# Kernel tuning notes

Hardware: AMD Instinct MI355X
Metric: run time of the kernel (lower is better)

## Reference

```python
import jax, jax.numpy as jnp
import numpy as np

B, N, IN_DIM, HID, K = 16, 1024, 512, 256, 3
ALPHA = 0.2  # leaky relu slope
NEG = -9e15  # mask value from original code (-9000000000000000.0)


def setup_inputs() -> dict:
    key = jax.random.key(0)
    ks = jax.random.split(key, 10)
    adj = (jax.random.uniform(ks[0], (B, 3, N, N)) < 0.01).astype(jnp.float32)
    inputs = jax.random.normal(ks[1], (B, N, IN_DIM), dtype=jnp.float32)
    s = 0.07
    W = jax.random.normal(ks[2], (3, K, IN_DIM, HID), dtype=jnp.float32) * s
    # attention vector a [2F,1] split into a1 (for h_i) and a2 (for h_j)
    a1 = jax.random.normal(ks[3], (3, K, HID), dtype=jnp.float32) * s
    a2 = jax.random.normal(ks[4], (3, K, HID), dtype=jnp.float32) * s
    Ww = jax.random.normal(ks[5], (HID, 100), dtype=jnp.float32) * s
    bw = jnp.zeros((100,), dtype=jnp.float32)
    Wc = jax.random.normal(ks[6], (100, 1), dtype=jnp.float32) * s
    return {"adj": adj, "inputs": inputs, "W": W, "a1": a1, "a2": a2,
            "Ww": Ww, "bw": bw, "Wc": Wc}


def _gat(adjp, inputs, W_, a1_, a2_):
    # h = X W : [B,N,F]
    h = jnp.einsum('bni,if->bnf', inputs, W_)
    # e_ij = leakyrelu(a1.h_i + a2.h_j) -- equivalent to the original
    # cat([h_i, h_j]) @ a without materializing the [B,N,N,2F] tensor
    f1 = h @ a1_  # [B,N]
    f2 = h @ a2_  # [B,N]
    e = jax.nn.leaky_relu(f1[:, :, None] + f2[:, None, :], ALPHA)
    att = jax.nn.softmax(jnp.where(adjp > 0, e, NEG), axis=2)
    # (dropout on attention is identity in eval mode)
    return jnp.einsum('bnm,bmf->bnf', att, h)


def reference(adj, inputs, W, a1, a2, Ww, bw, Wc):
    k_layers = W.shape[1]
    # powers[t] holds adj_t^(k+1) for layer k (matmuls(adj, k))
    powers = [adj[:, t] for t in range(3)]
    layer_list = []
    for k in range(k_layers):
        out = 0.0
        for t in range(3):
            out = out + _gat(powers[t], inputs, W[t, k], a1[t, k], a2[t, k])
        layer_list.append(out)
        if k + 1 < k_layers:
            powers = [jnp.matmul(p, adj[:, t]) for t, p in enumerate(powers)]
    H = jnp.stack(layer_list, axis=2)  # [B,N,K,F]
    s = jnp.tanh(H @ Ww + bw) @ Wc     # [B,N,K,1]
    vs = jax.nn.softmax(s[..., 0], axis=2)  # [B,N,K]
    return jnp.einsum('bnk,bnkf->bnf', vs, H)
```

## Files before the change

kernel.cpp:

```cpp
#include <hip/hip_runtime.h>


typedef unsigned long long u64;
typedef __attribute__((ext_vector_type(4))) float f32x4;
typedef __attribute__((ext_vector_type(8))) short bf16x8;

#define NEGF (-9.0e15f)
#define L2E 1.44269504f

__device__ __forceinline__ float fexp2(float x){
#if __has_builtin(__builtin_amdgcn_exp2f)
  return __builtin_amdgcn_exp2f(x);
#else
  return exp2f(x);
#endif
}
__device__ __forceinline__ float frcp(float x){
#if __has_builtin(__builtin_amdgcn_rcpf)
  return __builtin_amdgcn_rcpf(x);
#else
  return 1.0f/x;
#endif
}
__device__ __forceinline__ unsigned short f2bf(float x){
  union { float f; unsigned u; } a; a.f = x;
  unsigned r = a.u + 0x7FFFu + ((a.u >> 16) & 1u);
  return (unsigned short)(r >> 16);
}
__device__ __forceinline__ unsigned pack_bf16x2(float lo, float hi){
  union { float f; unsigned u; } a, b; a.f = lo; b.f = hi;
  unsigned ul = a.u + 0x8000u, uh = b.u + 0x8000u;
#if __has_builtin(__builtin_amdgcn_perm)
  return __builtin_amdgcn_perm(uh, ul, 0x07060302u);
#else
  return (ul >> 16) | (uh & 0xFFFF0000u);
#endif
}
__device__ __forceinline__ float tanh_fast(float x){
  float e = fexp2(x * 2.885390082f);
  return 1.0f - 2.0f*frcp(e + 1.0f);
}
__device__ __forceinline__ void async_cp16(void* lds, const void* g){
  __builtin_amdgcn_global_load_lds(
      (const __attribute__((address_space(1))) unsigned int*)g,
      (__attribute__((address_space(3))) unsigned int*)lds, 16, 0, 0);
}


__global__ __launch_bounds__(256) void k_prep(
    const float* __restrict__ W, const float* __restrict__ a1,
    const float* __restrict__ a2, unsigned short* __restrict__ Wb,
    const float* __restrict__ X, unsigned short* __restrict__ Xs,
    const float* __restrict__ adj, u64* __restrict__ mbA0, u64* __restrict__ mbT)
{
  if (blockIdx.x < 608) {
    int idx = blockIdx.x*256 + threadIdx.x;
    if (idx >= 64*2432) return;
    int c = idx % 2432, g = idx / 2432;
    unsigned short o[8];
    if (c < 2304) {
      int s = c >> 8, f = c & 255, t = s % 3, klq = s / 3;
      const float* wp = W + ((size_t)(t*3 + klq)*512)*256 + f;
#pragma unroll
      for (int e = 0; e < 8; ++e) o[e] = f2bf(wp[(size_t)(g*8 + e)*256]);
    } else if (c < 2322) {
      return;
    } else {
#pragma unroll
      for (int e = 0; e < 8; ++e) o[e] = 0;
    }
    ushort4 lo, hi;
    lo.x=o[0]; lo.y=o[1]; lo.z=o[2]; lo.w=o[3];
    hi.x=o[4]; hi.y=o[5]; hi.z=o[6]; hi.w=o[7];
    ushort4* dst = (ushort4*)(Wb + (size_t)idx*8);
    dst[0] = lo; dst[1] = hi;
  } else if (blockIdx.x < 896) {
    int wv = (blockIdx.x - 608)*4 + (threadIdx.x >> 6);
    int lane = threadIdx.x & 63;
    int c2 = wv >> 6, g = wv & 63;
    int s = c2 >> 1, t = s % 3, klq = s / 3;
    const float* av = ((c2 & 1) ? a2 : a1) + (t*3 + klq)*256;
    const float* wp = W + ((size_t)(t*3 + klq)*512)*256;
    float4 avv = *(const float4*)(av + lane*4);
    unsigned short o[8];
#pragma unroll
    for (int e = 0; e < 8; ++e) {
      float4 wv4 = *(const float4*)(wp + (size_t)(g*8 + e)*256 + lane*4);
      float p = wv4.x*avv.x + wv4.y*avv.y + wv4.z*avv.z + wv4.w*avv.w;
#pragma unroll
      for (int off = 32; off; off >>= 1) p += __shfl_xor(p, off);
      o[e] = f2bf(p);
    }
    if (lane == 0) {
      ushort4 lo, hi;
      lo.x=o[0]; lo.y=o[1]; lo.z=o[2]; lo.w=o[3];
      hi.x=o[4]; hi.y=o[5]; hi.z=o[6]; hi.w=o[7];
      ushort4* dst = (ushort4*)(Wb + (size_t)(g*2432 + 2304 + c2)*8);
      dst[0] = lo; dst[1] = hi;
    }
  } else if (blockIdx.x < 4992) {
    int idx = (blockIdx.x - 896)*256 + threadIdx.x;
    int bn = idx & 16383, g = idx >> 14;
    const float* xp = X + (size_t)bn*512 + g*8;
    ushort4 lo, hi;
    lo.x=f2bf(xp[0]); lo.y=f2bf(xp[1]); lo.z=f2bf(xp[2]); lo.w=f2bf(xp[3]);
    hi.x=f2bf(xp[4]); hi.y=f2bf(xp[5]); hi.z=f2bf(xp[6]); hi.w=f2bf(xp[7]);
    ushort4* dst = (ushort4*)(Xs + (size_t)idx*8);
    dst[0] = lo; dst[1] = hi;
  } else {
    int gw = (blockIdx.x - 4992)*4 + (threadIdx.x >> 6);
    int lane = threadIdx.x & 63;
#pragma unroll
    for (int r = 0; r < 2; ++r) {
      int row = gw*2 + r;
      int i = row & 1023, bt = row >> 10;
      int t = bt % 3, b = bt / 3;
      int sb = t*16 + b;
      const float* ap = adj + (size_t)row*1024 + lane;
      u64 myw = 0;
#pragma unroll
      for (int w = 0; w < 16; ++w) {
        u64 bal = __ballot(ap[w*64] > 0.0f);
        if (lane == w) myw = bal;
      }
      if (lane < 16) {
        mbA0[((size_t)sb*1024 + i)*16 + lane] = myw;
        mbT[((size_t)sb*16 + lane)*1024 + i] = myw;
      }
    }
  }
}

__global__ void k_boolmm(const u64* __restrict__ A, const u64* __restrict__ Bm,
                         u64* __restrict__ outA, u64* __restrict__ outT, int sbase)
{
  int tid = blockIdx.x*256 + threadIdx.x;
  int w = tid & 15, i = (tid >> 4) & 1023, tb = tid >> 14;
  const u64* Ar = A + ((size_t)tb*1024 + i)*16;
  const u64* Bb = Bm + (size_t)tb*16384;
  u64 acc = 0;
  for (int ww = 0; ww < 16; ++ww) {
    u64 aw = Ar[ww];
    while (aw) {
      int kk = __builtin_ctzll(aw);
      aw &= aw - 1;
      acc |= Bb[((size_t)(ww*64 + kk))*16 + w];
    }
  }
  if (outA) outA[((size_t)tb*1024 + i)*16 + w] = acc;
  int t = tb >> 4, bq = tb & 15;
  outT[(((size_t)(sbase + t)*16 + bq)*16 + w)*1024 + i] = acc;
}


__global__ __launch_bounds__(256) void k_gemm_h(
    const unsigned short* __restrict__ Xs, const unsigned short* __restrict__ Wb,
    unsigned short* __restrict__ hsw, float* __restrict__ fbuf,
    float* __restrict__ G1p, float* __restrict__ G2p)
{
  __shared__ unsigned short Asl[8*132*8 + 8];
  __shared__ unsigned short Bsl[8*132*8 + 8];
  const int tid = threadIdx.x, lane = tid & 63, wid = tid >> 6;
  int vb = blockIdx.x;
  int xc = vb & 7, mrest = vb >> 3;
  int mt = xc + 8*(mrest/19), nt = mrest % 19;
  const int M0 = mt << 7, N0 = nt << 7;
  const int wr = (wid >> 1) << 6, wc = (wid & 1) << 6;
  const int me = lane & 15;
  f32x4 acc[4][4] = {};
  for (int ks64 = 0; ks64 < 8; ++ks64) {
    __syncthreads();
#pragma unroll
    for (int c = 0; c < 4; ++c) {
      int chunk = wid*4 + c, g = chunk >> 1, hh = chunk & 1;
      int ldsoff = (g*132 + hh*64)*8;
      const unsigned short* gpA = Xs + ((size_t)(ks64*8 + g)*16384 + (M0 + hh*64 + lane))*8;
      async_cp16(Asl + ldsoff, gpA);
      const unsigned short* gpB = Wb + ((size_t)(ks64*8 + g)*2432 + (N0 + hh*64 + lane))*8;
      async_cp16(Bsl + ldsoff, gpB);
    }
    __syncthreads();
#pragma unroll
    for (int ks32 = 0; ks32 < 2; ++ks32) {
      const int kg = ks32*4 + (lane >> 4);
      bf16x8 afr[4], bfr[4];
#pragma unroll
      for (int rb = 0; rb < 4; ++rb)
        afr[rb] = *(const bf16x8*)(Asl + (kg*132 + wr + rb*16 + me)*8);
#pragma unroll
      for (int cb = 0; cb < 4; ++cb)
        bfr[cb] = *(const bf16x8*)(Bsl + (kg*132 + wc + cb*16 + me)*8);
#pragma unroll
      for (int rb = 0; rb < 4; ++rb)
#pragma unroll
        for (int cb = 0; cb < 4; ++cb)
          acc[rb][cb] = __builtin_amdgcn_mfma_f32_16x16x32_bf16(afr[rb], bfr[cb], acc[rb][cb], 0, 0, 0);
    }
  }
  const int quad = lane >> 4;
#pragma unroll
  for (int rb = 0; rb < 4; ++rb) {
    int jbase = M0 + wr + rb*16 + quad*4;
    int bidx = jbase >> 10, jn = jbase & 1023;
#pragma unroll
    for (int cb = 0; cb < 4; ++cb) {
      int c = N0 + wc + cb*16 + me;
      f32x4 v = acc[rb][cb];
      if (c < 2304) {
        int s = c >> 8, f = c & 255;
        ushort4 pk;
        pk.x = f2bf(v[0]); pk.y = f2bf(v[1]); pk.z = f2bf(v[2]); pk.w = f2bf(v[3]);
        *(ushort4*)(hsw + (size_t)s*4194304 + (size_t)bidx*262144 + ((jn>>3)*256 + f)*8 + (jn&7)) = pk;
      } else if (c < 2322) {
        int c2 = c - 2304, s = c2 >> 1, wh = c2 & 1;
        f32x4 vL = v * L2E;
        if (wh == 0) {
          *(f32x4*)(fbuf + (size_t)s*16384 + jbase) = vL;
        } else {
          f32x4 g1v, g2v;
#pragma unroll
          for (int k = 0; k < 4; ++k) {
            g1v[k] = fexp2(vL[k]);
            g2v[k] = fexp2(0.2f*vL[k]);
          }
          *(f32x4*)(G1p + (size_t)s*16384 + jbase) = g1v;
          *(f32x4*)(G2p + (size_t)s*16384 + jbase) = g2v;
        }
      }
    }
  }
}


__global__ __launch_bounds__(256) void k_rowl(
    const u64* __restrict__ mbT, const float* __restrict__ fbuf,
    const float* __restrict__ G1p, const float* __restrict__ G2p,
    float* __restrict__ rowR1, float* __restrict__ rowR2,
    float* __restrict__ rowRT, float* __restrict__ rowZr)
{
  int lane = threadIdx.x & 63;
  for (int gw = blockIdx.x*4 + (threadIdx.x >> 6); gw < 147456; gw += 18432) {
    int i = gw & 1023, sb = gw >> 10;
    int b = sb & 15, s = sb >> 4;

    const float* g1q = G1p + (size_t)s*16384 + b*1024 + lane*16;
    const float* g2q = G2p + (size_t)s*16384 + b*1024 + lane*16;
    float4 a0 = *(const float4*)(g1q);
    float4 a1 = *(const float4*)(g1q + 4);
    float4 a2 = *(const float4*)(g1q + 8);
    float4 a3 = *(const float4*)(g1q + 12);
    float4 c0 = *(const float4*)(g2q);
    float4 c1 = *(const float4*)(g2q + 4);
    float4 c2 = *(const float4*)(g2q + 8);
    float4 c3 = *(const float4*)(g2q + 12);
    float g1e[16] = {a0.x,a0.y,a0.z,a0.w, a1.x,a1.y,a1.z,a1.w,
                     a2.x,a2.y,a2.z,a2.w, a3.x,a3.y,a3.z,a3.w};
    float g2e[16] = {c0.x,c0.y,c0.z,c0.w, c1.x,c1.y,c1.z,c1.w,
                     c2.x,c2.y,c2.z,c2.w, c3.x,c3.y,c3.z,c3.w};

    u64 word = mbT[(size_t)sb*16384 + (size_t)(lane >> 2)*1024 + i];
    unsigned fld = (unsigned)(word >> ((lane & 3)*16)) & 0xFFFFu;

    float f1i = fbuf[(size_t)s*16384 + b*1024 + i];
    float RT = fexp2(-f1i);

    float S1 = 0.0f, S2 = 0.0f;
#pragma unroll
    for (int e = 0; e < 16; ++e) {
      unsigned m32 = (unsigned)(((int)(fld << (31 - e))) >> 31);
      float t1 = __uint_as_float(__float_as_uint(g1e[e]) & m32);
      float t2 = __uint_as_float(__float_as_uint(g2e[e]) & m32);
      bool c = (g1e[e] >= RT);
      S1 += c ? t1 : 0.0f;
      S2 += c ? 0.0f : t2;
    }
#pragma unroll
    for (int off = 32; off; off >>= 1) {
      S1 += __shfl_xor(S1, off);
      S2 += __shfl_xor(S2, off);
    }
    if (lane == 0) {
      float EF1 = fexp2(f1i);
      float EF2 = fexp2(0.2f*f1i);
      float l = __builtin_fmaf(EF1, S1, EF2*S2);
      float rinv = frcp(l);
      rowR1[gw] = EF1*rinv;
      rowR2[gw] = EF2*rinv;
      rowRT[gw] = RT;
      rowZr[gw] = (l == 0.0f) ? 0.0009765625f : 0.0f;
    }
  }
}


__global__ __launch_bounds__(256, 3) void k_attgemm(
    const unsigned short* __restrict__ hsw,
    const float* __restrict__ G1p, const float* __restrict__ G2p,
    const float* __restrict__ rowR1, const float* __restrict__ rowR2,
    const float* __restrict__ rowRT, const float* __restrict__ rowZr,
    const u64* __restrict__ mbT, float* __restrict__ H32)
{
  __shared__ unsigned short Bts[2*8192];
  const int tid = threadIdx.x, lane = tid & 63, wid = tid >> 6;
  const int me = lane & 15, quad = lane >> 4;
  int vb = blockIdx.x;
  int mt = vb / 48, g = vb % 48;
  int kl = g >> 4, b = g & 15;
  const int i0w = mt*64 + wid*16;
  const int ir0 = i0w + me;
  const unsigned short* hbase = hsw + (size_t)(kl*3)*4194304 + (size_t)b*262144;
  const float* g1b = G1p + (size_t)(kl*3)*16384 + b*1024;
  const float* g2b = G2p + (size_t)(kl*3)*16384 + b*1024;
  const float* R1b = rowR1 + ((kl*3)*16 + b)*1024;
  const float* R2b = rowR2 + ((kl*3)*16 + b)*1024;
  const float* RTb = rowRT + ((kl*3)*16 + b)*1024;
  const float* Zrb = rowZr + ((kl*3)*16 + b)*1024;
  const u64* mb = mbT + (size_t)((kl*3)*16 + b)*16384;

  float R1v, R2v, RTv;
  unsigned Zru;
  f32x4 acc[16] = {};

  {
    const unsigned short* hstage = hbase + wid*2048;
    unsigned short* lb = Bts + wid*2048;
#pragma unroll
    for (int c = 0; c < 4; ++c)
      async_cp16(lb + c*512, hstage + c*512 + lane*8);
  }
  u64 mw = mb[ir0];
  u64 nm = 0;

  for (int it = 0; it < 96; ++it) {
    const int tt = it >> 5, kk = it & 1;
    const int st = (it >> 1) & 15;
    if ((it & 31) == 0) {
      R1v = R1b[tt*16384 + ir0];
      R2v = R2b[tt*16384 + ir0];
      RTv = RTb[tt*16384 + ir0];
      Zru = __float_as_uint(Zrb[tt*16384 + ir0]);
    }
    if (!kk && it) mw = nm;

    __syncthreads();

    if (it + 1 < 96) {
      int nx = it + 1;
      int nt2 = nx >> 5, ns = (nx >> 1) & 15, nk = nx & 1;
      const unsigned short* hstage = hbase + (size_t)nt2*4194304 + ns*16384 + (nk*4 + wid)*2048;
      unsigned short* lb = Bts + nk*8192 + wid*2048;
#pragma unroll
      for (int c = 0; c < 4; ++c)
        async_cp16(lb + c*512, hstage + c*512 + lane*8);
    }
    if (kk && it + 1 < 96) {
      int gid = (it + 1) >> 1;
      int nt2 = gid >> 4, ns = gid & 15;
      nm = mb[(size_t)nt2*262144 + ns*1024 + ir0];
    }

    const int joff = tt*16384 + st*64 + kk*32 + quad*8;
    float4 ga = *(const float4*)(g1b + joff);
    float4 gb4 = *(const float4*)(g1b + joff + 4);
    float4 ha = *(const float4*)(g2b + joff);
    float4 hb4 = *(const float4*)(g2b + joff + 4);
    float g1e[8] = {ga.x, ga.y, ga.z, ga.w, gb4.x, gb4.y, gb4.z, gb4.w};
    float g2e[8] = {ha.x, ha.y, ha.z, ha.w, hb4.x, hb4.y, hb4.z, hb4.w};

    const int kloc = kk*32 + quad*8;
    unsigned mby = (unsigned)((mw >> kloc) & 0xFFull);
    union { bf16x8 v; unsigned u[4]; } ua;
#pragma unroll
    for (int p = 0; p < 4; ++p) {
      float p0, p1;
      {
        const int e = 2*p;
        bool c = (g1e[e] >= RTv);
        float pu = (c ? g1e[e] : g2e[e]) * (c ? R1v : R2v);
        unsigned m32 = (unsigned)(((int)(mby << (31 - e))) >> 31);
        p0 = __uint_as_float((__float_as_uint(pu) & m32) | Zru);
      }
      {
        const int e = 2*p + 1;
        bool c = (g1e[e] >= RTv);
        float pu = (c ? g1e[e] : g2e[e]) * (c ? R1v : R2v);
        unsigned m32 = (unsigned)(((int)(mby << (31 - e))) >> 31);
        p1 = __uint_as_float((__float_as_uint(pu) & m32) | Zru);
      }
      ua.u[p] = pack_bf16x2(p0, p1);
    }
    const unsigned short* bbase = Bts + kk*8192 + quad*2048;
#pragma unroll
    for (int cb = 0; cb < 16; ++cb) {
      bf16x8 bf = *(const bf16x8*)(bbase + (cb*16 + me)*8);
      acc[cb] = __builtin_amdgcn_mfma_f32_16x16x32_bf16(ua.v, bf, acc[cb], 0, 0, 0);
    }
  }

  {
    int io = i0w + quad*4;
#pragma unroll
    for (int cb = 0; cb < 16; ++cb) {
      int f = cb*16 + me;
      float* hp = H32 + (((size_t)b*1024 + io)*3 + kl)*256 + f;
#pragma unroll
      for (int r = 0; r < 4; ++r)
        hp[(size_t)r*768] = acc[cb][r];
    }
  }
}


__global__ __launch_bounds__(384) void k_scorecomb(
    const float* __restrict__ H32, const float* __restrict__ Ww,
    const float* __restrict__ bwv, const float* __restrict__ Wcv,
    float* __restrict__ out)
{
  __shared__ unsigned short Bs[8*7*64*8];
  __shared__ float bwL[128], WcL[128];
  __shared__ float svL[96];
  const int tid = threadIdx.x, lane = tid & 63, wid = tid >> 6;
  const int me = lane & 15, quad = lane >> 4;
  for (int idx = tid; idx < 3584; idx += 384) {
    int kk = idx / 448, rem = idx % 448;
    int cb = rem >> 6, l = rem & 63;
    int n = cb*16 + (l & 15);
    int kbase = kk*32 + (l >> 4)*8;
    ushort4 lo, hi;
    if (n < 100) {
      const float* wp = Ww + (size_t)kbase*100 + n;
      lo.x = f2bf(wp[0]);   lo.y = f2bf(wp[100]); lo.z = f2bf(wp[200]); lo.w = f2bf(wp[300]);
      hi.x = f2bf(wp[400]); hi.y = f2bf(wp[500]); hi.z = f2bf(wp[600]); hi.w = f2bf(wp[700]);
    } else {
      lo.x=lo.y=lo.z=lo.w=0; hi.x=hi.y=hi.z=hi.w=0;
    }
    ushort4* dst = (ushort4*)(Bs + (size_t)idx*8);
    dst[0] = lo; dst[1] = hi;
  }
  if (tid < 128) {
    bwL[tid] = (tid < 100) ? bwv[tid] : 0.0f;
    WcL[tid] = (tid < 100) ? Wcv[tid] : 0.0f;
  }
  __syncthreads();

  const int row0 = blockIdx.x*96 + wid*16;
  const float* Arow = H32 + (size_t)(row0 + me)*256;
  f32x4 acc[7] = {};
#pragma unroll
  for (int kk = 0; kk < 8; ++kk) {
    const float* ap = Arow + kk*32 + quad*8;
    float4 a0 = *(const float4*)(ap);
    float4 a1 = *(const float4*)(ap + 4);
    union { bf16x8 v; unsigned u[4]; } ua;
    ua.u[0] = pack_bf16x2(a0.x, a0.y);
    ua.u[1] = pack_bf16x2(a0.z, a0.w);
    ua.u[2] = pack_bf16x2(a1.x, a1.y);
    ua.u[3] = pack_bf16x2(a1.z, a1.w);
#pragma unroll
    for (int cb = 0; cb < 7; ++cb) {
      bf16x8 bf = *(const bf16x8*)(Bs + ((size_t)(kk*7 + cb)*64 + lane)*8);
      acc[cb] = __builtin_amdgcn_mfma_f32_16x16x32_bf16(ua.v, bf, acc[cb], 0, 0, 0);
    }
  }
#pragma unroll
  for (int r = 0; r < 4; ++r) {
    float contrib = 0.0f;
#pragma unroll
    for (int cb = 0; cb < 7; ++cb) {
      int col = cb*16 + me;
      contrib += tanh_fast(acc[cb][r] + bwL[col]) * WcL[col];
    }
    contrib += __shfl_xor(contrib, 1);
    contrib += __shfl_xor(contrib, 2);
    contrib += __shfl_xor(contrib, 4);
    contrib += __shfl_xor(contrib, 8);
    if (me == 0) svL[wid*16 + quad*4 + r] = contrib;
  }
  __syncthreads();

  const int bn0 = blockIdx.x*32;
  for (int idx = tid; idx < 2048; idx += 384) {
    int fq = idx & 63, bl = idx >> 6;
    int bn = bn0 + bl;
    float s0 = svL[bl*3], s1 = svL[bl*3+1], s2 = svL[bl*3+2];
    float mm = fmaxf(s0, fmaxf(s1, s2));
    float e0 = fexp2((s0-mm)*L2E), e1 = fexp2((s1-mm)*L2E), e2 = fexp2((s2-mm)*L2E);
    float inv = frcp(e0 + e1 + e2);
    const f32x4* h0 = (const f32x4*)(H32 + (size_t)bn*768) + fq;
    const f32x4* h1 = (const f32x4*)(H32 + (size_t)bn*768 + 256) + fq;
    const f32x4* h2 = (const f32x4*)(H32 + (size_t)bn*768 + 512) + fq;
    f32x4 r = (e0*(*h0) + e1*(*h1) + e2*(*h2))*inv;
    *((f32x4*)out + (size_t)bn*64 + fq) = r;
  }
}


extern "C" void kernel_launch(void* const* d_in, const int* in_sizes, int n_in,
                              void* d_out, int out_size, void* d_ws, size_t ws_size,
                              hipStream_t stream) {
  const float* adj = (const float*)d_in[0];
  const float* X   = (const float*)d_in[1];
  const float* W   = (const float*)d_in[2];
  const float* a1  = (const float*)d_in[3];
  const float* a2  = (const float*)d_in[4];
  const float* Ww  = (const float*)d_in[5];
  const float* bw  = (const float*)d_in[6];
  const float* Wc  = (const float*)d_in[7];
  float* out = (float*)d_out;
  char* ws = (char*)d_ws;

  unsigned short* Xs  = (unsigned short*)(ws + 0);
  unsigned short* Wb  = (unsigned short*)(ws + 16777216);
  float* H32          = (float*)(ws + 0);
  unsigned short* hsw = (unsigned short*)(ws + 50331648);
  u64* mbA            = (u64*)(ws + 125829120);
  float* rowR1        = (float*)(ws + 125829120);
  float* rowR2        = (float*)(ws + 126418944);
  float* rowRT        = (float*)(ws + 127008768);
  float* rowZr        = (float*)(ws + 127598592);
  u64* mbT            = (u64*)(ws + 138412032);
  float* fbuf         = (float*)(ws + 157286400);
  float* G1p          = (float*)(ws + 158466048);
  float* G2p          = (float*)(ws + 159055872);

  k_prep<<<11136, 256, 0, stream>>>(W, a1, a2, Wb, X, Xs, adj, mbA, mbT);
  k_boolmm<<<3072, 256, 0, stream>>>(mbA, mbA, mbA + 786432, mbT, 3);
  k_boolmm<<<3072, 256, 0, stream>>>(mbA, mbA + 786432, (u64*)nullptr, mbT, 6);
  k_gemm_h<<<2432, 256, 0, stream>>>(Xs, Wb, hsw, fbuf, G1p, G2p);
  k_rowl<<<4608, 256, 0, stream>>>(mbT, fbuf, G1p, G2p, rowR1, rowR2, rowRT, rowZr);
  k_attgemm<<<768, 256, 0, stream>>>(hsw, G1p, G2p, rowR1, rowR2, rowRT, rowZr, mbT, H32);
  k_scorecomb<<<512, 384, 0, stream>>>(H32, Ww, bw, Wc, out);
}
```

Measured before the change: 383.1 us.

## Double-buffer LDS tiles in k_gemm_h to overlap global loads with MFMA

Replaces the single-buffered 64-wide K loop in the projection GEMM with a two-buffer pipeline over 32-wide K slices. The next slice is issued as async copies into the alternate LDS buffer while the current slice feeds the MFMAs. This removes one barrier per step and is meant to hide global load latency behind compute. The cost is twice as many loop iterations with less MFMA work per barrier, and the barrier still waits on outstanding copies.

After: 391.9 us. 1.02x slower.

```diff
diff --git a/kernel.cpp b/kernel.cpp
--- a/kernel.cpp
+++ b/kernel.cpp
@@ -158,46 +158,53 @@
     unsigned short* __restrict__ hsw, float* __restrict__ fbuf,
     float* __restrict__ G1p, float* __restrict__ G2p)
 {
-  __shared__ unsigned short Asl[8*132*8 + 8];
-  __shared__ unsigned short Bsl[8*132*8 + 8];
+  __shared__ unsigned short Asl[2][4*132*8];
+  __shared__ unsigned short Bsl[2][4*132*8];
   const int tid = threadIdx.x, lane = tid & 63, wid = tid >> 6;
   int vb = blockIdx.x;
   int xc = vb & 7, mrest = vb >> 3;
   int mt = xc + 8*(mrest/19), nt = mrest % 19;
   const int M0 = mt << 7, N0 = nt << 7;
   const int wr = (wid >> 1) << 6, wc = (wid & 1) << 6;
-  const int me = lane & 15;
+  const int me = lane & 15, quad = lane >> 4;
   f32x4 acc[4][4] = {};
-  for (int ks64 = 0; ks64 < 8; ++ks64) {
+
+#pragma unroll
+  for (int c = 0; c < 2; ++c) {
+    int chunk = wid*2 + c, g = chunk >> 1, hh = chunk & 1;
+    int ldsoff = (g*132 + hh*64)*8;
+    async_cp16(&Asl[0][ldsoff], Xs + ((size_t)g*16384 + (M0 + hh*64 + lane))*8);
+    async_cp16(&Bsl[0][ldsoff], Wb + ((size_t)g*2432 + (N0 + hh*64 + lane))*8);
+  }
+
+  for (int it = 0; it < 16; ++it) {
     __syncthreads();
-#pragma unroll
-    for (int c = 0; c < 4; ++c) {
-      int chunk = wid*4 + c, g = chunk >> 1, hh = chunk & 1;
-      int ldsoff = (g*132 + hh*64)*8;
-      const unsigned short* gpA = Xs + ((size_t)(ks64*8 + g)*16384 + (M0 + hh*64 + lane))*8;
-      async_cp16(Asl + ldsoff, gpA);
-      const unsigned short* gpB = Wb + ((size_t)(ks64*8 + g)*2432 + (N0 + hh*64 + lane))*8;
-      async_cp16(Bsl + ldsoff, gpB);
-    }
-    __syncthreads();
-#pragma unroll
-    for (int ks32 = 0; ks32 < 2; ++ks32) {
-      const int kg = ks32*4 + (lane >> 4);
-      bf16x8 afr[4], bfr[4];
-#pragma unroll
-      for (int rb = 0; rb < 4; ++rb)
-        afr[rb] = *(const bf16x8*)(Asl + (kg*132 + wr + rb*16 + me)*8);
+    if (it + 1 < 16) {
+      int nb = (it + 1) & 1;
+#pragma unroll
+      for (int c = 0; c < 2; ++c) {
+        int chunk = wid*2 + c, g = chunk >> 1, hh = chunk & 1;
+        int kb = (it + 1)*4 + g;
+        int ldsoff = (g*132 + hh*64)*8;
+        async_cp16(&Asl[nb][ldsoff], Xs + ((size_t)kb*16384 + (M0 + hh*64 + lane))*8);
+        async_cp16(&Bsl[nb][ldsoff], Wb + ((size_t)kb*2432 + (N0 + hh*64 + lane))*8);
+      }
+    }
+    const int cb2 = it & 1;
+    bf16x8 afr[4], bfr[4];
+#pragma unroll
+    for (int rb = 0; rb < 4; ++rb)
+      afr[rb] = *(const bf16x8*)(&Asl[cb2][(quad*132 + wr + rb*16 + me)*8]);
+#pragma unroll
+    for (int cb = 0; cb < 4; ++cb)
+      bfr[cb] = *(const bf16x8*)(&Bsl[cb2][(quad*132 + wc + cb*16 + me)*8]);
+#pragma unroll
+    for (int rb = 0; rb < 4; ++rb)
 #pragma unroll
       for (int cb = 0; cb < 4; ++cb)
-        bfr[cb] = *(const bf16x8*)(Bsl + (kg*132 + wc + cb*16 + me)*8);
-#pragma unroll
-      for (int rb = 0; rb < 4; ++rb)
-#pragma unroll
-        for (int cb = 0; cb < 4; ++cb)
-          acc[rb][cb] = __builtin_amdgcn_mfma_f32_16x16x32_bf16(afr[rb], bfr[cb], acc[rb][cb], 0, 0, 0);
-    }
-  }
-  const int quad = lane >> 4;
+        acc[rb][cb] = __builtin_amdgcn_mfma_f32_16x16x32_bf16(afr[rb], bfr[cb], acc[rb][cb], 0, 0, 0);
+  }
+
 #pragma unroll
   for (int rb = 0; rb < 4; ++rb) {
     int jbase = M0 + wr + rb*16 + quad*4;
```
